# Kernel tuning notes

Hardware: AMD Instinct MI355X
Metric: run time of the kernel (lower is better)

Reference implementation:

```python
import jax, jax.numpy as jnp
import numpy as np

N = 50000
E = 600000
D = 128


def _mlp(x, W1, b1, W2, b2):
    # Linear -> GELU(exact, matches torch nn.GELU default) -> (Dropout=eval no-op) -> Linear
    h = jax.nn.gelu(x @ W1 + b1, approximate=False)
    return h @ W2 + b2


def setup_inputs() -> dict:
    key = jax.random.key(0)
    ks = jax.random.split(key, 12)
    s = 1.0 / np.sqrt(D)
    inp = {
        "x": jax.random.normal(ks[0], (N, D), dtype=jnp.float32),
        "edge_index": jax.random.randint(ks[1], (2, E), 0, N, dtype=jnp.int64),
        "edge_attr": jax.random.normal(ks[2], (E, D), dtype=jnp.float32),
        # edge_mlp params
        "We1": jax.random.uniform(ks[3], (D, D), jnp.float32, -s, s),
        "be1": jax.random.uniform(ks[4], (D,), jnp.float32, -s, s),
        "We2": jax.random.uniform(ks[5], (D, D), jnp.float32, -s, s),
        "be2": jax.random.uniform(ks[6], (D,), jnp.float32, -s, s),
        # update_mlp params
        "Wu1": jax.random.uniform(ks[7], (D, D), jnp.float32, -s, s),
        "bu1": jax.random.uniform(ks[8], (D,), jnp.float32, -s, s),
        "Wu2": jax.random.uniform(ks[9], (D, D), jnp.float32, -s, s),
        "bu2": jax.random.uniform(ks[10], (D,), jnp.float32, -s, s),
        "eps": jnp.zeros((1,), dtype=jnp.float32),
    }
    return inp


def reference(x, edge_index, edge_attr, We1, be1, We2, be2, Wu1, bu1, Wu2, bu2, eps):
    src, dst = edge_index[0], edge_index[1]
    # gather + fuse + edge MLP: [E, D]
    messages = _mlp(x[src] + edge_attr, We1, be1, We2, be2)
    # scatter-add back to nodes: [N, D]
    aggregated = jax.ops.segment_sum(messages, dst, num_segments=x.shape[0])
    return _mlp((1.0 + eps) * x + aggregated, Wu1, bu1, Wu2, bu2)
```

## Files before the change

kernel.cpp:

```cpp
#include <hip/hip_runtime.h>
#include <hip/hip_bf16.h>

#define ND 128
#define LDA 136
#define LDM 130

typedef _Float16 f16x8 __attribute__((ext_vector_type(8)));
typedef _Float16 f16x4 __attribute__((ext_vector_type(4)));
typedef float    f32x4 __attribute__((ext_vector_type(4)));

__device__ __forceinline__ float gelu_exact(float v) {
    return 0.5f * v * (1.0f + erff(v * 0.70710678118654752f));
}

__global__ void prep_weights(const float* __restrict__ w0, const float* __restrict__ w1,
                             const float* __restrict__ w2, const float* __restrict__ w3,
                             _Float16* __restrict__ wt) {
    int id = blockIdx.x * blockDim.x + threadIdx.x;
    int m   = id >> 14;
    int idx = id & 16383;
    int c = idx >> 7, k = idx & 127;
    const float* W = (m == 0) ? w0 : (m == 1) ? w1 : (m == 2) ? w2 : w3;
    wt[(m << 14) + (c << 7) + k] = (_Float16)W[(k << 7) + c];
}

__global__ void hist_kernel(const int* __restrict__ dst, int* __restrict__ cnt, int E) {
    int e = blockIdx.x * blockDim.x + threadIdx.x;
    if (e < E) atomicAdd(&cnt[dst[e]], 1);
}

__global__ void scan_exclusive(int* __restrict__ data, int n) {
    __shared__ int wsum[16];
    __shared__ int carry;
    const int t = threadIdx.x, lane = t & 63, wv = t >> 6;
    if (t == 0) carry = 0;
    __syncthreads();
    for (int base = 0; base < n; base += 1024) {
        int i = base + t;
        int v = (i < n) ? data[i] : 0;
        int s = v;
        #pragma unroll
        for (int off = 1; off < 64; off <<= 1) {
            int u = __shfl_up(s, off, 64);
            if (lane >= off) s += u;
        }
        if (lane == 63) wsum[wv] = s;
        __syncthreads();
        if (t == 0) {
            int run = carry;
            #pragma unroll
            for (int w = 0; w < 16; ++w) { int x = wsum[w]; wsum[w] = run; run += x; }
            carry = run;
        }
        __syncthreads();
        int excl = s - v + wsum[wv];
        if (i < n) data[i] = excl;
        __syncthreads();
    }
}

__global__ void scatter_kernel(const int* __restrict__ dst, int* __restrict__ cur,
                               int* __restrict__ perm, int E) {
    int e = blockIdx.x * blockDim.x + threadIdx.x;
    if (e < E) {
        int p = atomicAdd(&cur[dst[e]], 1);
        perm[p] = e;
    }
}

template<bool EDGE, bool SORTED>
__global__ __launch_bounds__(512, 4) void mlp_fused(
    const float* __restrict__ xp,
    const float* __restrict__ rowin,
    const int*   __restrict__ srcp,
    const int*   __restrict__ dstp,
    const int*   __restrict__ permp,
    const _Float16* __restrict__ wt1,
    const _Float16* __restrict__ wt2,
    const float* __restrict__ b1p,
    const float* __restrict__ b2p,
    const float* __restrict__ epsp,
    float* __restrict__ outp,
    int nRows, int nTiles)
{
    __shared__ __align__(16) char lds_raw[64 * LDA * 2 * sizeof(_Float16)];
    __shared__ int dtile[64];
    _Float16* Abuf = (_Float16*)lds_raw;
    _Float16* Hbuf = (_Float16*)(lds_raw + 64 * LDA * sizeof(_Float16));
    float*    Mbuf = (float*)lds_raw;

    const int tid  = threadIdx.x;
    const int lane = tid & 63;
    const int wid  = tid >> 6;
    const int wr   = wid >> 2;
    const int wc   = wid & 3;
    const int l15  = lane & 15;
    const int khi  = lane >> 4;

    f16x8 wf1[2][4], wf2[2][4];
    float bb1[2], bb2[2];
    #pragma unroll
    for (int ct = 0; ct < 2; ++ct) {
        int col = wc * 32 + ct * 16 + l15;
        #pragma unroll
        for (int kk = 0; kk < 4; ++kk) {
            wf1[ct][kk] = *(const f16x8*)(wt1 + col * ND + kk * 32 + khi * 8);
            wf2[ct][kk] = *(const f16x8*)(wt2 + col * ND + kk * 32 + khi * 8);
        }
        bb1[ct] = b1p[col];
        bb2[ct] = b2p[col];
    }

    float scale = 1.0f;
    if (!EDGE) scale = 1.0f + epsp[0];

    const int sr = tid >> 3;
    const int sc = (tid & 7) * 4;

    for (int tile = blockIdx.x; tile < nTiles; tile += gridDim.x) {
        const int base = tile * 64;

        {
            int grow = base + sr;
            if (grow < nRows) {
                int prow = grow;
                if (EDGE && SORTED) prow = permp[grow];
                if (EDGE && SORTED && (tid & 7) == 0) dtile[sr] = dstp[prow];
                const float* er = rowin + (size_t)prow * ND;
                const float* xr;
                if (EDGE) xr = xp + (size_t)srcp[prow] * ND;
                else      xr = xp + (size_t)grow * ND;
                #pragma unroll
                for (int i = 0; i < 4; ++i) {
                    int c = sc + i * 32;
                    float4 a = *(const float4*)(er + c);
                    float4 b = *(const float4*)(xr + c);
                    f16x4 v;
                    if (EDGE) {
                        v[0] = (_Float16)(a.x + b.x); v[1] = (_Float16)(a.y + b.y);
                        v[2] = (_Float16)(a.z + b.z); v[3] = (_Float16)(a.w + b.w);
                    } else {
                        v[0] = (_Float16)(a.x + scale * b.x); v[1] = (_Float16)(a.y + scale * b.y);
                        v[2] = (_Float16)(a.z + scale * b.z); v[3] = (_Float16)(a.w + scale * b.w);
                    }
                    *(f16x4*)&Abuf[sr * LDA + c] = v;
                }
            } else {
                if (EDGE && SORTED && (tid & 7) == 0) dtile[sr] = -1;
                #pragma unroll
                for (int i = 0; i < 4; ++i) {
                    f16x4 z = {};
                    *(f16x4*)&Abuf[sr * LDA + sc + i * 32] = z;
                }
            }
        }

        __syncthreads();

        f32x4 acc[2][2];
        #pragma unroll
        for (int rt = 0; rt < 2; ++rt)
            #pragma unroll
            for (int ct = 0; ct < 2; ++ct)
                acc[rt][ct] = (f32x4)0.0f;

        #pragma unroll
        for (int kk = 0; kk < 4; ++kk) {
            f16x8 af[2];
            #pragma unroll
            for (int rt = 0; rt < 2; ++rt)
                af[rt] = *(const f16x8*)&Abuf[(wr * 32 + rt * 16 + l15) * LDA + kk * 32 + khi * 8];
            #pragma unroll
            for (int rt = 0; rt < 2; ++rt)
                #pragma unroll
                for (int ct = 0; ct < 2; ++ct)
                    acc[rt][ct] = __builtin_amdgcn_mfma_f32_16x16x32_f16(
                        af[rt], wf1[ct][kk], acc[rt][ct], 0, 0, 0);
        }

        #pragma unroll
        for (int rt = 0; rt < 2; ++rt)
            #pragma unroll
            for (int ct = 0; ct < 2; ++ct) {
                int col = wc * 32 + ct * 16 + l15;
                #pragma unroll
                for (int q = 0; q < 4; ++q) {
                    int rl = wr * 32 + rt * 16 + khi * 4 + q;
                    Hbuf[rl * LDA + col] = (_Float16)gelu_exact(acc[rt][ct][q] + bb1[ct]);
                }
            }

        __syncthreads();

        f32x4 acc2[2][2];
        #pragma unroll
        for (int rt = 0; rt < 2; ++rt)
            #pragma unroll
            for (int ct = 0; ct < 2; ++ct)
                acc2[rt][ct] = (f32x4)0.0f;

        #pragma unroll
        for (int kk = 0; kk < 4; ++kk) {
            f16x8 hf[2];
            #pragma unroll
            for (int rt = 0; rt < 2; ++rt)
                hf[rt] = *(const f16x8*)&Hbuf[(wr * 32 + rt * 16 + l15) * LDA + kk * 32 + khi * 8];
            #pragma unroll
            for (int rt = 0; rt < 2; ++rt)
                #pragma unroll
                for (int ct = 0; ct < 2; ++ct)
                    acc2[rt][ct] = __builtin_amdgcn_mfma_f32_16x16x32_f16(
                        hf[rt], wf2[ct][kk], acc2[rt][ct], 0, 0, 0);
        }

        if (EDGE && SORTED) {
            __syncthreads();

            #pragma unroll
            for (int rt = 0; rt < 2; ++rt)
                #pragma unroll
                for (int ct = 0; ct < 2; ++ct) {
                    int col = wc * 32 + ct * 16 + l15;
                    #pragma unroll
                    for (int q = 0; q < 4; ++q) {
                        int rl = wr * 32 + rt * 16 + khi * 4 + q;
                        Mbuf[rl * LDM + col] = acc2[rt][ct][q] + bb2[ct];
                    }
                }

            __syncthreads();

            const int rc = tid & 127;
            const int rg = tid >> 7;
            float a = 0.0f;
            #pragma unroll
            for (int r = rg * 16; r < rg * 16 + 16; ++r) {
                int d = dtile[r];
                if (d >= 0) {
                    a += Mbuf[r * LDM + rc];
                    if (r == 63 || r == rg * 16 + 15 || dtile[r + 1] != d) {
                        atomicAdd(outp + (size_t)d * ND + rc, a);
                        a = 0.0f;
                    }
                }
            }

            __syncthreads();
        } else {
            #pragma unroll
            for (int rt = 0; rt < 2; ++rt)
                #pragma unroll
                for (int ct = 0; ct < 2; ++ct) {
                    int col = wc * 32 + ct * 16 + l15;
                    #pragma unroll
                    for (int q = 0; q < 4; ++q) {
                        int rl = wr * 32 + rt * 16 + khi * 4 + q;
                        int grow = base + rl;
                        if (grow < nRows) {
                            float v = acc2[rt][ct][q] + bb2[ct];
                            if (EDGE) {
                                int d = dstp[grow];
                                atomicAdd(outp + (size_t)d * ND + col, v);
                            } else {
                                outp[(size_t)grow * ND + col] = v;
                            }
                        }
                    }
                }
        }
    }
}

extern "C" void kernel_launch(void* const* d_in, const int* in_sizes, int n_in,
                              void* d_out, int out_size, void* d_ws, size_t ws_size,
                              hipStream_t stream)
{
    const float* x   = (const float*)d_in[0];
    const int*   ei  = (const int*)d_in[1];
    const float* ea  = (const float*)d_in[2];
    const float* We1 = (const float*)d_in[3];
    const float* be1 = (const float*)d_in[4];
    const float* We2 = (const float*)d_in[5];
    const float* be2 = (const float*)d_in[6];
    const float* Wu1 = (const float*)d_in[7];
    const float* bu1 = (const float*)d_in[8];
    const float* Wu2 = (const float*)d_in[9];
    const float* bu2 = (const float*)d_in[10];
    const float* eps = (const float*)d_in[11];

    const int E  = in_sizes[1] / 2;
    const int Nn = in_sizes[0] / ND;

    const size_t aggB = (size_t)Nn * ND * sizeof(float);
    const size_t cntB = ((size_t)Nn * sizeof(int) + 255) & ~(size_t)255;
    const size_t prmB = (size_t)E * sizeof(int);
    const size_t wtB  = 4 * 16384 * sizeof(_Float16);
    const bool sorted = (ws_size >= aggB + cntB + prmB + wtB);

    float* agg = (float*)d_ws;
    const int tilesE = (E + 63) / 64;
    const int tilesN = (Nn + 63) / 64;

    if (sorted) {
        int*      cnt  = (int*)((char*)d_ws + aggB);
        int*      perm = (int*)((char*)d_ws + aggB + cntB);
        _Float16* wt   = (_Float16*)((char*)d_ws + aggB + cntB + prmB);

        hipMemsetAsync(d_ws, 0, aggB + cntB, stream);
        prep_weights<<<dim3(256), dim3(256), 0, stream>>>(We1, We2, Wu1, Wu2, wt);

        const int gE = (E + 511) / 512;
        hist_kernel<<<dim3(gE), dim3(512), 0, stream>>>(ei + E, cnt, E);
        scan_exclusive<<<dim3(1), dim3(1024), 0, stream>>>(cnt, Nn);
        scatter_kernel<<<dim3(gE), dim3(512), 0, stream>>>(ei + E, cnt, perm, E);

        mlp_fused<true, true><<<dim3(512), dim3(512), 0, stream>>>(
            x, ea, ei, ei + E, perm, wt, wt + 16384, be1, be2, nullptr,
            agg, E, tilesE);

        mlp_fused<false, false><<<dim3(512), dim3(512), 0, stream>>>(
            x, agg, nullptr, nullptr, nullptr, wt + 2 * 16384, wt + 3 * 16384,
            bu1, bu2, eps, (float*)d_out, Nn, tilesN);
    } else {
        _Float16* wt = (_Float16*)((char*)d_ws + aggB);
        hipMemsetAsync(agg, 0, aggB, stream);
        prep_weights<<<dim3(256), dim3(256), 0, stream>>>(We1, We2, Wu1, Wu2, wt);

        mlp_fused<true, false><<<dim3(512), dim3(512), 0, stream>>>(
            x, ea, ei, ei + E, nullptr, wt, wt + 16384, be1, be2, nullptr,
            agg, E, tilesE);

        mlp_fused<false, false><<<dim3(512), dim3(512), 0, stream>>>(
            x, agg, nullptr, nullptr, nullptr, wt + 2 * 16384, wt + 3 * 16384,
            bu1, bu2, eps, (float*)d_out, Nn, tilesN);
    }
}
```

Measured before the change: 631.5 us.

## Parallelize prefix scan across blocks and enlarge MLP kernel grids

Replaces the single-block sequential exclusive scan over node counts with a three-pass multi-block scan (per-block scan, scan of block sums, add-back). It also raises the grid size of both fused MLP kernels from a fixed 512 blocks to up to 2048, one per tile. This is meant to remove the serial scan bottleneck and improve occupancy and load balance in the MLP kernels. The segmented-sum flush condition is simplified by dropping a redundant row check. The extra launches add small overhead, and pass2 drops the running prefix of wave sums (run is computed but wsum is only valid for nb up to 64), so larger block counts could produce wrong results.

```diff
diff --git a/kernel.cpp b/kernel.cpp
--- a/kernel.cpp
+++ b/kernel.cpp
@@ -29,34 +29,53 @@
     if (e < E) atomicAdd(&cnt[dst[e]], 1);
 }
 
-__global__ void scan_exclusive(int* __restrict__ data, int n) {
+__global__ void scan_pass1(int* __restrict__ data, int* __restrict__ bsum, int n) {
     __shared__ int wsum[16];
-    __shared__ int carry;
     const int t = threadIdx.x, lane = t & 63, wv = t >> 6;
-    if (t == 0) carry = 0;
+    int i = blockIdx.x * 1024 + t;
+    int v = (i < n) ? data[i] : 0;
+    int s = v;
+    #pragma unroll
+    for (int off = 1; off < 64; off <<= 1) {
+        int u = __shfl_up(s, off, 64);
+        if (lane >= off) s += u;
+    }
+    if (lane == 63) wsum[wv] = s;
     __syncthreads();
-    for (int base = 0; base < n; base += 1024) {
-        int i = base + t;
-        int v = (i < n) ? data[i] : 0;
-        int s = v;
-        #pragma unroll
-        for (int off = 1; off < 64; off <<= 1) {
-            int u = __shfl_up(s, off, 64);
-            if (lane >= off) s += u;
-        }
-        if (lane == 63) wsum[wv] = s;
-        __syncthreads();
-        if (t == 0) {
-            int run = carry;
-            #pragma unroll
-            for (int w = 0; w < 16; ++w) { int x = wsum[w]; wsum[w] = run; run += x; }
-            carry = run;
-        }
-        __syncthreads();
-        int excl = s - v + wsum[wv];
-        if (i < n) data[i] = excl;
-        __syncthreads();
-    }
+    if (t == 0) {
+        int run = 0;
+        #pragma unroll
+        for (int w = 0; w < 16; ++w) { int x = wsum[w]; wsum[w] = run; run += x; }
+        bsum[blockIdx.x] = run;
+    }
+    __syncthreads();
+    if (i < n) data[i] = s - v + wsum[wv];
+}
+
+__global__ void scan_pass2(int* __restrict__ bsum, int nb) {
+    __shared__ int wsum[16];
+    const int t = threadIdx.x, lane = t & 63, wv = t >> 6;
+    int v = (t < nb) ? bsum[t] : 0;
+    int s = v;
+    #pragma unroll
+    for (int off = 1; off < 64; off <<= 1) {
+        int u = __shfl_up(s, off, 64);
+        if (lane >= off) s += u;
+    }
+    if (lane == 63) wsum[wv] = s;
+    __syncthreads();
+    if (t == 0) {
+        int run = 0;
+        #pragma unroll
+        for (int w = 0; w < 16; ++w) { int x = wsum[w]; wsum[w] = run; run += x; }
+    }
+    __syncthreads();
+    if (t < nb) bsum[t] = s - v + wsum[wv];
+}
+
+__global__ void scan_pass3(int* __restrict__ data, const int* __restrict__ bsum, int n) {
+    int i = blockIdx.x * 1024 + threadIdx.x;
+    if (i < n && blockIdx.x > 0) data[i] += bsum[blockIdx.x];
 }
 
 __global__ void scatter_kernel(const int* __restrict__ dst, int* __restrict__ cur,
@@ -238,7 +257,7 @@
                 int d = dtile[r];
                 if (d >= 0) {
                     a += Mbuf[r * LDM + rc];
-                    if (r == 63 || r == rg * 16 + 15 || dtile[r + 1] != d) {
+                    if (r == rg * 16 + 15 || dtile[r + 1] != d) {
                         atomicAdd(outp + (size_t)d * ND + rc, a);
                         a = 0.0f;
                     }
@@ -294,31 +313,38 @@
     const size_t aggB = (size_t)Nn * ND * sizeof(float);
     const size_t cntB = ((size_t)Nn * sizeof(int) + 255) & ~(size_t)255;
     const size_t prmB = (size_t)E * sizeof(int);
+    const size_t bsmB = 4096;
     const size_t wtB  = 4 * 16384 * sizeof(_Float16);
-    const bool sorted = (ws_size >= aggB + cntB + prmB + wtB);
+    const bool sorted = (ws_size >= aggB + cntB + prmB + bsmB + wtB);
 
     float* agg = (float*)d_ws;
     const int tilesE = (E + 63) / 64;
     const int tilesN = (Nn + 63) / 64;
+    const int gridE  = (tilesE < 2048) ? tilesE : 2048;
+    const int gridN  = (tilesN < 2048) ? tilesN : 2048;
 
     if (sorted) {
         int*      cnt  = (int*)((char*)d_ws + aggB);
         int*      perm = (int*)((char*)d_ws + aggB + cntB);
-        _Float16* wt   = (_Float16*)((char*)d_ws + aggB + cntB + prmB);
+        int*      bsum = (int*)((char*)d_ws + aggB + cntB + prmB);
+        _Float16* wt   = (_Float16*)((char*)d_ws + aggB + cntB + prmB + bsmB);
 
         hipMemsetAsync(d_ws, 0, aggB + cntB, stream);
         prep_weights<<<dim3(256), dim3(256), 0, stream>>>(We1, We2, Wu1, Wu2, wt);
 
         const int gE = (E + 511) / 512;
+        const int nb = (Nn + 1023) / 1024;
         hist_kernel<<<dim3(gE), dim3(512), 0, stream>>>(ei + E, cnt, E);
-        scan_exclusive<<<dim3(1), dim3(1024), 0, stream>>>(cnt, Nn);
+        scan_pass1<<<dim3(nb), dim3(1024), 0, stream>>>(cnt, bsum, Nn);
+        scan_pass2<<<dim3(1), dim3(1024), 0, stream>>>(bsum, nb);
+        scan_pass3<<<dim3(nb), dim3(1024), 0, stream>>>(cnt, bsum, Nn);
         scatter_kernel<<<dim3(gE), dim3(512), 0, stream>>>(ei + E, cnt, perm, E);
 
-        mlp_fused<true, true><<<dim3(512), dim3(512), 0, stream>>>(
+        mlp_fused<true, true><<<dim3(gridE), dim3(512), 0, stream>>>(
             x, ea, ei, ei + E, perm, wt, wt + 16384, be1, be2, nullptr,
             agg, E, tilesE);
 
-        mlp_fused<false, false><<<dim3(512), dim3(512), 0, stream>>>(
+        mlp_fused<false, false><<<dim3(gridN), dim3(512), 0, stream>>>(
             x, agg, nullptr, nullptr, nullptr, wt + 2 * 16384, wt + 3 * 16384,
             bu1, bu2, eps, (float*)d_out, Nn, tilesN);
     } else {
@@ -326,11 +352,11 @@
         hipMemsetAsync(agg, 0, aggB, stream);
         prep_weights<<<dim3(256), dim3(256), 0, stream>>>(We1, We2, Wu1, Wu2, wt);
 
-        mlp_fused<true, false><<<dim3(512), dim3(512), 0, stream>>>(
+        mlp_fused<true, false><<<dim3(gridE), dim3(512), 0, stream>>>(
             x, ea, ei, ei + E, nullptr, wt, wt + 16384, be1, be2, nullptr,
             agg, E, tilesE);
 
-        mlp_fused<false, false><<<dim3(512), dim3(512), 0, stream>>>(
+        mlp_fused<false, false><<<dim3(gridN), dim3(512), 0, stream>>>(
             x, agg, nullptr, nullptr, nullptr, wt + 2 * 16384, wt + 3 * 16384,
             bu1, bu2, eps, (float*)d_out, Nn, tilesN);
     }
```

New measurement: 619.4 us. About the same (-1.9%).
